# Optimization experiments

Measured on AMD Instinct MI355X. Metric: run time of the kernel, lower is better.

Reference implementation:

```python
import jax, jax.numpy as jnp
import numpy as np

EPS_OT = 0.05   # sinkhorn epsilon
ITERS = 3       # sinkhorn iterations
NH = 8          # attention heads


def _l2norm(x, axis):
    return x / jnp.maximum(jnp.linalg.norm(x, axis=axis, keepdims=True), 1e-12)


def _conv(x, w, pad):
    return jax.lax.conv_general_dilated(
        x, w, (1, 1), ((pad, pad), (pad, pad)),
        dimension_numbers=("NCHW", "OIHW", "NCHW"))


def _head(x, w1, b1, g, beta, w2, b2):
    # Conv3x3 -> BatchNorm (train-mode batch stats) -> ReLU -> Conv1x1
    h = _conv(x, w1, 1) + b1[None, :, None, None]
    mu = jnp.mean(h, (0, 2, 3), keepdims=True)
    var = jnp.var(h, (0, 2, 3), keepdims=True)
    h = jax.nn.relu((h - mu) / jnp.sqrt(var + 1e-5) * g[None, :, None, None]
                    + beta[None, :, None, None])
    return jnp.einsum("oc,bchw->bohw", w2, h) + b2[None, :, None, None]


def setup_inputs() -> dict:
    key = jax.random.key(0)
    ks = jax.random.split(key, 20)
    B, C, H, W, TD = 8, 256, 48, 48, 512
    s = 0.02
    f32 = jnp.float32
    d = {
        "img_feat": jax.random.normal(ks[0], (B, C, H, W), f32),
        "txt_feat": jax.random.normal(ks[1], (B, TD), f32),
        "density_map": jax.random.uniform(ks[2], (B, 1, H, W), f32),
        "tp_w": s * jax.random.normal(ks[3], (C, TD), f32), "tp_b": jnp.zeros((C,), f32),
        "wq": s * jax.random.normal(ks[4], (C, C), f32), "bq": jnp.zeros((C,), f32),
        "wk": s * jax.random.normal(ks[5], (C, C), f32), "bk": jnp.zeros((C,), f32),
        "wv": s * jax.random.normal(ks[6], (C, C), f32), "bv": jnp.zeros((C,), f32),
        "wo": s * jax.random.normal(ks[7], (C, C), f32), "bo": jnp.zeros((C,), f32),
        "ln_g": jnp.ones((C,), f32), "ln_b": jnp.zeros((C,), f32),
        "op_w": s * jax.random.normal(ks[8], (C, C), f32), "op_b": jnp.zeros((C,), f32),
        "h1_w": s * jax.random.normal(ks[9], (C // 2, C, 3, 3), f32), "h1_b": jnp.zeros((C // 2,), f32),
        "h_bn_g": jnp.ones((C // 2,), f32), "h_bn_b": jnp.zeros((C // 2,), f32),
        "h2_w": s * jax.random.normal(ks[10], (2, C // 2), f32), "h2_b": jnp.zeros((2,), f32),
        "v1_w": s * jax.random.normal(ks[11], (C // 2, C, 3, 3), f32), "v1_b": jnp.zeros((C // 2,), f32),
        "v_bn_g": jnp.ones((C // 2,), f32), "v_bn_b": jnp.zeros((C // 2,), f32),
        "v2_w": s * jax.random.normal(ks[12], (2, C // 2), f32), "v2_b": jnp.zeros((2,), f32),
        "temperature": 0.07 * jnp.ones((1,), f32),
        "spatial_weight": 0.1 * jnp.ones((1,), f32),
    }
    return d


def reference(img_feat, txt_feat, density_map, tp_w, tp_b, wq, bq, wk, bk,
              wv, bv, wo, bo, ln_g, ln_b, op_w, op_b, h1_w, h1_b, h_bn_g,
              h_bn_b, h2_w, h2_b, v1_w, v1_b, v_bn_g, v_bn_b, v2_w, v2_b,
              temperature, spatial_weight):
    B, C, H, W = img_feat.shape
    N = H * W
    hd = C // NH

    # ---- text projection (single text token) ----
    txt_emb = txt_feat @ tp_w.T + tp_b                      # [B,C]

    # ---- cross attention: query = pixels, key/value = 1 text token ----
    img_flat = img_feat.reshape(B, C, N).transpose(0, 2, 1)  # [B,N,C]
    q = (img_flat @ wq.T + bq).reshape(B, N, NH, hd)
    k = (txt_emb @ wk.T + bk).reshape(B, 1, NH, hd)
    v = (txt_emb @ wv.T + bv).reshape(B, 1, NH, hd)
    scores = jnp.einsum("bnhd,bkhd->bhnk", q, k) / jnp.sqrt(jnp.float32(hd))
    attn = jax.nn.softmax(scores, axis=-1)                  # ones (k len = 1)
    ctx = jnp.einsum("bhnk,bkhd->bnhd", attn, v).reshape(B, N, C)
    attn_out = ctx @ wo.T + bo

    # ---- residual + layernorm ----
    x = img_flat + attn_out
    mu = jnp.mean(x, -1, keepdims=True)
    var = jnp.var(x, -1, keepdims=True)
    source_feat = (x - mu) / jnp.sqrt(var + 1e-5) * ln_g + ln_b   # [B,N,C]
    mod_img_feat = source_feat.transpose(0, 2, 1).reshape(B, C, H, W)

    # ---- target distribution q from density map ----
    target = jax.nn.relu(density_map.reshape(B, N)) + 1e-6
    q_dist = target / jnp.sum(target, axis=1, keepdims=True)

    # ---- source distribution p from cosine similarity ----
    img_n = _l2norm(mod_img_feat, 1)                        # [B,C,H,W]
    txt_n = _l2norm(txt_emb, 1)                             # [B,C]
    cos = jnp.sum(img_n * txt_n[:, :, None, None], axis=1).reshape(B, N)
    temp = jnp.clip(temperature, 0.01, None)                # [1]
    logits = cos / temp
    mask = (cos > 0.0).astype(jnp.float32)
    shifted = logits - jnp.max(logits, axis=1, keepdims=True)
    p_un = jnp.exp(shifted) * mask + 1e-8
    p = p_un / jnp.sum(p_un, axis=1, keepdims=True)

    # ---- cost matrix: feature + spatial ----
    src_n = _l2norm(source_feat, 2)                         # [B,N,C]
    feature_cost = 1.0 - jnp.einsum("bnc,bmc->bnm", src_n, src_n)
    gy, gx = jnp.meshgrid(jnp.linspace(0.0, 1.0, H), jnp.linspace(0.0, 1.0, W),
                          indexing="ij")
    coords = jnp.stack([gy, gx], -1).reshape(N, 2)
    d2 = jnp.sum((coords[:, None, :] - coords[None, :, :]) ** 2, -1)
    spatial_cost = jnp.sqrt(jnp.maximum(d2, 0.0)) / 1.41421356  # [N,N]
    cost = feature_cost + spatial_weight * spatial_cost[None]   # [B,N,N]

    # ---- log-domain Sinkhorn ----
    log_p = jnp.log(p + 1e-12)
    log_q = jnp.log(q_dist + 1e-12)
    f = jnp.zeros_like(p)
    g = jnp.zeros_like(q_dist)
    for _ in range(ITERS):
        f = EPS_OT * (log_p - jax.scipy.special.logsumexp(
            (g[:, None, :] - cost) / EPS_OT, axis=2))
        g = EPS_OT * (log_q - jax.scipy.special.logsumexp(
            (f[:, :, None] - cost) / EPS_OT, axis=1))
    T = jnp.exp((f[:, :, None] + g[:, None, :] - cost) / EPS_OT)

    # ---- transport features: T^T @ source ----
    fused = jnp.einsum("bnm,bnc->bmc", T, source_feat)      # [B,N,C]
    fused_feat = fused.transpose(0, 2, 1).reshape(B, C, H, W)

    out_feat = img_feat + (jnp.einsum("oc,bchw->bohw", op_w, fused_feat)
                           + op_b[None, :, None, None])
    heatmap_logits = _head(out_feat, h1_w, h1_b, h_bn_g, h_bn_b, h2_w, h2_b)
    hv_logits = _head(out_feat, v1_w, v1_b, v_bn_g, v_bn_b, v2_w, v2_b)
    return out_feat, heatmap_logits, hv_logits
```

## Files before the change

### kernel.cpp

```cpp
#include <hip/hip_runtime.h>
#include <hip/hip_bf16.h>

#define NTOK 2304
#define CCH  256
#define BB   8
#define NSPL 2

typedef __attribute__((ext_vector_type(4))) float f32x4;
typedef __attribute__((ext_vector_type(8))) short s16x8;
typedef __attribute__((ext_vector_type(8))) _Float16 h16x8;
typedef unsigned short u16;
typedef unsigned char u8;

__device__ __forceinline__ u16 f2bf(float x){
  union{float f; unsigned u;} v; v.f = x;
  unsigned r = v.u + 0x7fffu + ((v.u>>16)&1u);
  return (u16)(r>>16);
}
__device__ __forceinline__ float bf2f(u16 h){
  union{float f; unsigned u;} v; v.u = ((unsigned)h)<<16; return v.f;
}

#if __has_builtin(__builtin_amdgcn_cvt_f32_fp8) && __has_builtin(__builtin_amdgcn_cvt_pk_fp8_f32)
#define HWFP8 1
#else
#define HWFP8 0
#endif

__device__ __forceinline__ u8 enc8(float z){
  union{float f; unsigned u;} a; a.f = fabsf(z) * 0x1p-120f;
  unsigned u = a.u + 0x7FFFFu + ((a.u>>20)&1u);
  unsigned b = (u>>20)&0x7Fu;
  if (b > 0x7Eu) b = 0x7Eu;
  return (u8)(b | (z<0.f ? 0x80u : 0u));
}
__device__ __forceinline__ float dec8(unsigned b){
  union{unsigned u; float f;} w;
  w.u = ((b&0x80u)<<24) | ((b&0x7Fu)<<20);
  return w.f * 0x1p120f;
}

#if HWFP8
__device__ __forceinline__ float DEC8(unsigned w, int e){
  switch(e & 3){
    case 0:  return __builtin_amdgcn_cvt_f32_fp8((int)w, 0);
    case 1:  return __builtin_amdgcn_cvt_f32_fp8((int)w, 1);
    case 2:  return __builtin_amdgcn_cvt_f32_fp8((int)w, 2);
    default: return __builtin_amdgcn_cvt_f32_fp8((int)w, 3);
  }
}
__device__ __forceinline__ unsigned pack4(float z0,float z1,float z2,float z3){
  int v = __builtin_amdgcn_cvt_pk_fp8_f32(z0, z1, 0, false);
  v = __builtin_amdgcn_cvt_pk_fp8_f32(z2, z3, v, true);
  return (unsigned)v;
}
#else
__device__ __forceinline__ float DEC8(unsigned w, int e){
  return dec8((w>>(8*(e&3)))&0xFFu);
}
__device__ __forceinline__ unsigned pack4(float z0,float z1,float z2,float z3){
  return (unsigned)enc8(z0) | ((unsigned)enc8(z1)<<8) |
         ((unsigned)enc8(z2)<<16) | ((unsigned)enc8(z3)<<24);
}
#endif

__device__ __forceinline__ int swz512(int row, int b){ return row*512 + (b ^ ((row&7)<<4)); }
__device__ __forceinline__ int swz128(int row, int b){ return row*128 + (b ^ ((row&7)<<4)); }
__device__ __forceinline__ int swz64 (int row, int b){ return row*64  + (b ^ ((row&3)<<4)); }

__device__ __forceinline__ void gl_lds16(const void* g, void* l){
  __builtin_amdgcn_global_load_lds(
      (const __attribute__((address_space(1))) unsigned int*)g,
      (__attribute__((address_space(3))) unsigned int*)l, 16, 0, 0);
}

struct CanonArgs {
  const void* src[31];
  int n[31];
  int off[31];
};

__global__ void k_detect(const u16* probe, int* flag){
  if (threadIdx.x==0){
    int cnt=0;
    for (int i=0;i<16;++i){
      unsigned e = (probe[2*i]>>7)&0xFFu;
      if (e>=100u && e<=140u) ++cnt;
    }
    *flag = (cnt>=14)?1:0;
  }
}

__global__ __launch_bounds__(256) void k_canon(CanonArgs a, float* dst, const int* flag, int nt){
  int t = blockIdx.y;
  if (t>=nt) return;
  int n = a.n[t];
  const void* s = a.src[t];
  float* d = dst + a.off[t];
  bool isbf = (*flag)!=0;
  int n4 = n >> 2;
  for (int i = blockIdx.x*256+threadIdx.x; i < n4; i += gridDim.x*256){
    if (isbf){
      ushort4 v = ((const ushort4*)s)[i];
      float4 o; o.x=bf2f(v.x); o.y=bf2f(v.y); o.z=bf2f(v.z); o.w=bf2f(v.w);
      ((float4*)d)[i] = o;
    } else {
      ((float4*)d)[i] = ((const float4*)s)[i];
    }
  }
  int base = n4<<2;
  int rem = n - base;
  int i = blockIdx.x*256+threadIdx.x;
  if (i < rem)
    d[base+i] = isbf ? bf2f(((const u16*)s)[base+i]) : ((const float*)s)[base+i];
}

__global__ __launch_bounds__(256) void k_zero(float* p, int n4){
  int i = blockIdx.x*256+threadIdx.x;
  if (i < n4) ((float4*)p)[i] = (float4){0.f,0.f,0.f,0.f};
}

__global__ __launch_bounds__(256) void k_txt(const float* txt, const float* tpw, const float* tpb,
    const float* wv, const float* bv, const float* wo, const float* bo, float* TXTN, float* AVEC){
  int b=blockIdx.x, t=threadIdx.x;
  __shared__ float sT[512];
  __shared__ float sE[256];
  __shared__ float sV[256];
  __shared__ float red[4];
  sT[t]      = txt[b*512+t];
  sT[t+256]  = txt[b*512+256+t];
  __syncthreads();
  float acc = tpb[t];
  const float* wr = tpw + (size_t)t*512;
  for (int k=0;k<512;++k) acc = fmaf(sT[k], wr[k], acc);
  sE[t] = acc;
  float ss = acc*acc;
  for (int d=1; d<64; d<<=1) ss += __shfl_xor(ss, d);
  if ((t&63)==0) red[t>>6] = ss;
  __syncthreads();
  float nrm = sqrtf(red[0]+red[1]+red[2]+red[3]);
  TXTN[b*256+t] = acc / fmaxf(nrm, 1e-12f);
  float av = bv[t];
  const float* wvr = wv + (size_t)t*256;
  for (int k=0;k<256;++k) av = fmaf(sE[k], wvr[k], av);
  sV[t] = av;
  __syncthreads();
  float ao = bo[t];
  const float* wor = wo + (size_t)t*256;
  for (int k=0;k<256;++k) ao = fmaf(sV[k], wor[k], ao);
  AVEC[b*256+t] = ao;
}

__global__ __launch_bounds__(256) void k_lnfuse(const float* img, const float* AVEC, const float* lng,
    const float* lnb, const float* TXTN, u16* SF, u16* SN, float* COS){
  int b=blockIdx.y, n0=blockIdx.x*32, t=threadIdx.x;
  __shared__ float xt[32][256];
  float av = AVEC[b*256+t];
  const float* ip = img + ((size_t)b*256 + t)*NTOK + n0;
  #pragma unroll
  for (int j4=0;j4<8;++j4){
    float4 v = *(const float4*)(ip + j4*4);
    xt[j4*4+0][t]=v.x+av; xt[j4*4+1][t]=v.y+av; xt[j4*4+2][t]=v.z+av; xt[j4*4+3][t]=v.w+av;
  }
  int wv_=t>>6, l=t&63;
  float lg[4], lb[4], tn[4];
  #pragma unroll
  for (int k=0;k<4;++k){ lg[k]=lng[l+64*k]; lb[k]=lnb[l+64*k]; tn[k]=TXTN[b*256+l+64*k]; }
  __syncthreads();
  for (int rr=0; rr<8; ++rr){
    int j = wv_*8+rr; int n = n0+j;
    float x[4]; float s=0.f, ss=0.f;
    #pragma unroll
    for (int k=0;k<4;++k){ float v=xt[j][l+64*k]; x[k]=v; s+=v; ss=fmaf(v,v,ss); }
    for (int d=1; d<64; d<<=1){ s += __shfl_xor(s,d); ss += __shfl_xor(ss,d); }
    float mu = s*(1.f/256.f);
    float var = ss*(1.f/256.f) - mu*mu;
    float rstd = rsqrtf(fmaxf(var,0.f)+1e-5f);
    float y[4]; float sy=0.f;
    #pragma unroll
    for (int k=0;k<4;++k){ y[k] = fmaf((x[k]-mu)*rstd, lg[k], lb[k]); sy = fmaf(y[k],y[k],sy); }
    for (int d=1; d<64; d<<=1) sy += __shfl_xor(sy,d);
    float rn = 1.f/fmaxf(sqrtf(sy),1e-12f);
    float cp = 0.f;
    size_t base = ((size_t)b*NTOK + n)*CCH;
    #pragma unroll
    for (int k=0;k<4;++k){
      float sv = y[k]*rn;
      SF[base + l+64*k] = f2bf(y[k]);
      SN[base + l+64*k] = f2bf(sv);
      cp = fmaf(sv, tn[k], cp);
    }
    for (int d=1; d<64; d<<=1) cp += __shfl_xor(cp,d);
    if (l==0) COS[b*NTOK+n] = cp;
  }
}

__global__ __launch_bounds__(256) void k_pqred(const float* COS, const float* den, const float* tmpp, float* PQS){
  int b=blockIdx.x, t=threadIdx.x;
  __shared__ float red[256];
  float temp = fmaxf(tmpp[0], 0.01f);
  float mx = -1e30f;
  for (int n=t; n<NTOK; n+=256) mx = fmaxf(mx, COS[b*NTOK+n]);
  red[t]=mx; __syncthreads();
  for (int o=128;o>0;o>>=1){ if (t<o) red[t]=fmaxf(red[t],red[t+o]); __syncthreads(); }
  float maxc = red[0]; __syncthreads();
  float sp=0.f, st=0.f;
  for (int n=t; n<NTOK; n+=256){
    float cv = COS[b*NTOK+n];
    sp += __expf((cv-maxc)/temp)*((cv>0.f)?1.f:0.f)+1e-8f;
    float dv = den[b*NTOK+n];
    st += fmaxf(dv,0.f)+1e-6f;
  }
  red[t]=sp; __syncthreads();
  for (int o=128;o>0;o>>=1){ if (t<o) red[t]+=red[t+o]; __syncthreads(); }
  sp = red[0]; __syncthreads();
  red[t]=st; __syncthreads();
  for (int o=128;o>0;o>>=1){ if (t<o) red[t]+=red[t+o]; __syncthreads(); }
  if (t==0){ PQS[b*4]=maxc; PQS[b*4+1]=sp; PQS[b*4+2]=red[0]; }
}

__global__ __launch_bounds__(256) void k_pqelem(const float* COS, const float* den, const float* tmpp,
    const float* PQS, float* LOGP, float* LOGQ, float* GV, float* CY, float* CX){
  int idx = blockIdx.x*256+threadIdx.x;
  float temp = fmaxf(tmpp[0], 0.01f);
  if (idx < BB*NTOK){
    int b = idx / NTOK;
    float maxc = PQS[b*4], sp = PQS[b*4+1], st = PQS[b*4+2];
    float cv = COS[idx];
    float pu = __expf((cv-maxc)/temp)*((cv>0.f)?1.f:0.f)+1e-8f;
    LOGP[idx] = logf(pu/sp + 1e-12f);
    float dv = den[idx];
    LOGQ[idx] = logf((fmaxf(dv,0.f)+1e-6f)/st + 1e-12f);
    GV[idx] = 0.f;
  }
  if (idx < NTOK){
    int h = idx/48, w = idx - h*48;
    CY[idx] = (float)h*(1.f/47.f);
    CX[idx] = (float)w*(1.f/47.f);
  }
}

__global__ __launch_bounds__(256) void k_packw(const float* h1w, const float* v1w, u16* W2P){
  int idx = blockIdx.x*256+threadIdx.x;
  int kc = idx >> 14;
  int rem = idx & 16383;
  int o = rem >> 6;
  int cl = rem & 63;
  int tap = kc >> 2;
  int c = ((kc&3)<<6) + cl;
  int head = o >> 7, oc = o & 127;
  const float* src = head ? v1w : h1w;
  W2P[idx] = f2bf(src[(oc*256 + c)*9 + tap]);
}

__global__ __launch_bounds__(256) void k_trans(const u16* SF, u16* SFT){
  int n0 = blockIdx.x*64, c0 = blockIdx.y*64, b = blockIdx.z;
  __shared__ u16 tl[64][68];
  int t = threadIdx.x;
  int nl = t>>3, c8 = (t&7)*8;
  #pragma unroll
  for (int p=0;p<2;++p){
    int n = nl + p*32;
    s16x8 v = *(const s16x8*)(SF + ((size_t)(b*NTOK + n0+n)*CCH + c0 + c8));
    #pragma unroll
    for (int e=0;e<8;++e) tl[c8+e][n] = (u16)v[e];
  }
  __syncthreads();
  int cl = t>>3, n8 = (t&7)*8;
  #pragma unroll
  for (int p=0;p<2;++p){
    int c = cl + p*32;
    union{ s16x8 v; u16 us[8]; } pk;
    #pragma unroll
    for (int e=0;e<8;++e){ int s = n8+e; pk.us[e] = tl[c][((s&3)<<4) | (s>>2)]; }
    *(s16x8*)(SFT + ((size_t)(b*CCH + c0+c)*NTOK + n0 + n8)) = pk.v;
  }
}

__global__ __launch_bounds__(256, 4) void k_cost(const u16* SN, const float* CY, const float* CX,
    const float* swp, u8* Z, float* PZ, int b_base){
  int zb = blockIdx.z, b = b_base + zb;
  int i0 = blockIdx.x*64, by = blockIdx.y, j0b = by*256;
  const u16* SNb = SN + (size_t)b*NTOK*CCH;
  u8* Zb = Z + (size_t)zb*NTOK*NTOK;
  __shared__ __align__(16) char Bs[64*512];
  int tid=threadIdx.x, w=tid>>6, l=tid&63, g4=l>>4, lc=l&15;
  float spw = swp[0]*(20.0f/1.41421356f);
  const u16* Arow = SNb + (size_t)(i0 + w*16 + lc)*CCH + g4*8;
  s16x8 af[8];
  #pragma unroll
  for (int ks=0; ks<8; ++ks) af[ks] = *(const s16x8*)(Arow + ks*32);
  int mrow = w*16 + g4*4;
  float cyi[4], cxi[4];
  #pragma unroll
  for (int r=0;r<4;++r){ int i = i0+mrow+r; cyi[r]=CY[i]; cxi[r]=CX[i]; }
  float Srow[4] = {0.f,0.f,0.f,0.f};
  for (int js=0; js<4; ++js){
    int j0 = j0b + js*64;
    __syncthreads();
    #pragma unroll
    for (int u=0; u<8; ++u){
      int row = u*8 + w*2 + (l>>5);
      int src = ((l&31)*16) ^ ((row&7)<<4);
      gl_lds16((const char*)(SNb + (size_t)(j0+row)*CCH) + src, Bs + u*4096 + w*1024);
    }
    __syncthreads();
    f32x4 acc[4];
    #pragma unroll
    for (int cf=0;cf<4;++cf) acc[cf] = (f32x4){0.f,0.f,0.f,0.f};
    #pragma unroll
    for (int ks=0; ks<8; ++ks){
      int kb = ks*64 + g4*16;
      #pragma unroll
      for (int cf=0; cf<4; ++cf){
        s16x8 bb = *(const s16x8*)(Bs + swz512(cf*16+lc, kb));
        acc[cf] = __builtin_amdgcn_mfma_f32_16x16x32_bf16(af[ks], bb, acc[cf], 0,0,0);
      }
    }
    float zf[4][4];
    #pragma unroll
    for (int cf=0; cf<4; ++cf){
      int j = j0 + cf*16 + lc;
      float cyj = CY[j], cxj = CX[j];
      #pragma unroll
      for (int r=0;r<4;++r){
        float dy = cyi[r]-cyj, dx = cxi[r]-cxj;
        zf[cf][r] = (acc[cf][r]-1.0f)*20.0f - spw*sqrtf(fmaf(dy,dy,dx*dx));
      }
    }
    size_t zrow = (size_t)(i0+mrow)*NTOK + j0 + lc*4;
    #pragma unroll
    for (int r=0;r<4;++r){
      unsigned pw = pack4(zf[0][r], zf[1][r], zf[2][r], zf[3][r]);
      Srow[r] += __expf(DEC8(pw,0)) + __expf(DEC8(pw,1))
               + __expf(DEC8(pw,2)) + __expf(DEC8(pw,3));
      *(unsigned*)(Zb + zrow + (size_t)r*NTOK) = pw;
    }
  }
  #pragma unroll
  for (int r=0;r<4;++r){
    float s = Srow[r];
    s += __shfl_xor(s,1); s += __shfl_xor(s,2); s += __shfl_xor(s,4); s += __shfl_xor(s,8);
    if (lc==0) PZ[(size_t)(zb*NTOK + i0 + mrow + r)*9 + by] = s;
  }
}

__global__ __launch_bounds__(256) void k_sinkred(const float* PZ, const float* LOGP, float* FV,
    int b_base, int zcnt){
  int idx = blockIdx.x*256 + threadIdx.x;
  if (idx >= zcnt*NTOK) return;
  int zb = idx / NTOK, row = idx - zb*NTOK, b = b_base + zb;
  const float* p = PZ + (size_t)idx*9;
  float s = 0.f;
  #pragma unroll
  for (int k=0;k<9;++k) s += p[k];
  FV[b*NTOK+row] = 0.05f*(LOGP[b*NTOK+row] - logf(s));
}

__global__ __launch_bounds__(256) void k_sinkZ(const u8* Z, const float* addv,
    const float* basev, float* outv, int b_base){
  int zb = blockIdx.y, b = b_base + zb, i0 = blockIdx.x*32;
  __shared__ float fs[NTOK];
  __shared__ float wm[4];
  int t = threadIdx.x;
  for (int j=t; j<NTOK; j+=256){
    int p = j & 63, tt = ((p&3)<<4) | (p>>2);
    fs[j] = addv[b*NTOK + (j & ~63) + tt]*20.f;
  }
  __syncthreads();
  float m = -1e30f;
  for (int j=t; j<NTOK; j+=256) m = fmaxf(m, fs[j]);
  #pragma unroll
  for (int d=1; d<64; d<<=1) m = fmaxf(m, __shfl_xor(m, d));
  if ((t&63)==0) wm[t>>6] = m;
  __syncthreads();
  float C = fmaxf(fmaxf(wm[0],wm[1]), fmaxf(wm[2],wm[3]));
  int rl = t>>3, q = t&7;
  int row = i0 + rl;
  const u8* zr = Z + ((size_t)zb*NTOK + row)*NTOK;
  float S = 0.f;
  for (int c0 = q*32; c0 < NTOK; c0 += 256){
    uint4 zA = *(const uint4*)(zr + c0);
    uint4 zB = *(const uint4*)(zr + c0 + 16);
    unsigned wd[8] = {zA.x,zA.y,zA.z,zA.w, zB.x,zB.y,zB.z,zB.w};
    float s32 = 0.f;
    #pragma unroll
    for (int k=0;k<8;++k)
      #pragma unroll
      for (int e=0;e<4;++e)
        s32 += __expf(fs[c0 + k*4 + e] + DEC8(wd[k], e) - C);
    S += s32;
  }
  #pragma unroll
  for (int d=1; d<8; d<<=1) S += __shfl_xor(S, d);
  if (q==0)
    outv[b*NTOK+row] = 0.05f*(basev[b*NTOK+row] - (C + logf(S)));
}

__global__ __launch_bounds__(256, 3) void k_applyT(const u8* Z, const u16* SFT, const float* FVv,
    const float* GVv, float* FUF, int b_base){
  int zb = blockIdx.z, b = b_base + zb, m0 = blockIdx.x*64;
  int sp = blockIdx.y;
  int nbeg = sp*(NTOK/NSPL), nend = nbeg + (NTOK/NSPL);
  __shared__ __align__(16) char WtL[64*128];
  __shared__ __align__(16) char BL[256*128];
  __shared__ float gs[64];
  __shared__ float sfv[NTOK/NSPL];
  int tid=threadIdx.x, w=tid>>6, l=tid&63, g4=l>>4, lc=l&15;
  if (tid<64) gs[tid] = GVv[b*NTOK+m0+tid]*20.f;
  const float* Fv = FVv + b*NTOK;
  for (int j=tid; j<NTOK/NSPL; j+=256){
    int jj = nbeg + j;
    int p = jj & 63, tt = ((p&3)<<4) | (p>>2);
    sfv[j] = Fv[(jj & ~63) + tt]*20.f;
  }
  const u8* Zb = Z + ((size_t)zb*NTOK + m0)*NTOK;
  const u16* SFTb = SFT + (size_t)b*CCH*NTOK;
  f32x4 acc[4][4];
  #pragma unroll
  for (int mf=0;mf<4;++mf)
    #pragma unroll
    for (int cf=0;cf<4;++cf) acc[mf][cf] = (f32x4){0.f,0.f,0.f,0.f};
  int zm = tid>>2, zq = (tid&3)*16;
  int lrow = l>>3;
  int lsrc = ((l&7)*16) ^ (lrow<<4);
  uint4 zwc = *(const uint4*)(Zb + (size_t)zm*NTOK + nbeg + zq);
  for (int n0=nbeg; n0<nend; n0+=64){
    __syncthreads();
    int nn = (n0+64 < nend) ? n0+64 : nbeg;
    uint4 zwn = *(const uint4*)(Zb + (size_t)zm*NTOK + nn + zq);
    #pragma unroll
    for (int u=0; u<8; ++u){
      int row = w*64 + u*8 + lrow;
      gl_lds16((const char*)(SFTb + (size_t)row*NTOK) + n0*2 + lsrc,
               BL + (w*64 + u*8)*128);
    }
    {
      float g20 = gs[zm];
      unsigned wd[4] = {zwc.x, zwc.y, zwc.z, zwc.w};
      union{ s16x8 v; u16 us[8]; } w0, w1;
      int sbase = n0 - nbeg + zq;
      #pragma unroll
      for (int col=0; col<16; ++col){
        float val = __expf(sfv[sbase+col] + g20 + DEC8(wd[col>>2], col&3));
        if (col < 8) w0.us[col] = f2bf(val); else w1.us[col-8] = f2bf(val);
      }
      *(s16x8*)(WtL + swz128(zm, zq*2)) = w0.v;
      *(s16x8*)(WtL + swz128(zm, zq*2+16)) = w1.v;
    }
    __syncthreads();
    #pragma unroll
    for (int kk=0; kk<2; ++kk){
      s16x8 a[4];
      #pragma unroll
      for (int mf=0;mf<4;++mf) a[mf] = *(const s16x8*)(WtL + swz128(mf*16+lc, kk*64 + g4*16));
      #pragma unroll
      for (int cf=0; cf<4; ++cf){
        s16x8 bb = *(const s16x8*)(BL + swz128(w*64+cf*16+lc, kk*64 + g4*16));
        #pragma unroll
        for (int mf=0; mf<4; ++mf)
          acc[mf][cf] = __builtin_amdgcn_mfma_f32_16x16x32_bf16(a[mf], bb, acc[mf][cf], 0,0,0);
      }
    }
    zwc = zwn;
  }
  float* FUb = FUF + (size_t)b*NTOK*CCH;
  #pragma unroll
  for (int mf=0; mf<4; ++mf)
    #pragma unroll
    for (int cf=0; cf<4; ++cf)
      #pragma unroll
      for (int r=0;r<4;++r){
        int m = m0 + mf*16 + g4*4 + r;
        int c = w*64 + cf*16 + lc;
        atomicAdd(&FUb[(size_t)m*CCH + c], acc[mf][cf][r]);
      }
}

__global__ __launch_bounds__(256) void k_opgemm(const float* FUF, const float* opw, const float* opb,
    const float* img, float* dout, u16* OFN){
  int b=blockIdx.y, n0=blockIdx.x*64;
  __shared__ __align__(16) char Am[64*512];
  __shared__ __align__(16) char Bw[256*64];
  int tid=threadIdx.x, w=tid>>6, l=tid&63, g4=l>>4, lc=l&15;
  const float* FUb = FUF + (size_t)b*NTOK*CCH;
  for (int ch=tid; ch<64*32; ch+=256){
    int r=ch>>5, c8=(ch&31)*8;
    const float* fp = FUb + (size_t)(n0+r)*CCH + c8;
    float4 v0 = *(const float4*)fp;
    float4 v1 = *(const float4*)(fp+4);
    union { s16x8 v; u16 us[8]; } pk;
    pk.us[0]=f2bf(v0.x); pk.us[1]=f2bf(v0.y); pk.us[2]=f2bf(v0.z); pk.us[3]=f2bf(v0.w);
    pk.us[4]=f2bf(v1.x); pk.us[5]=f2bf(v1.y); pk.us[6]=f2bf(v1.z); pk.us[7]=f2bf(v1.w);
    *(s16x8*)(Am + swz512(r, c8*2)) = pk.v;
  }
  f32x4 acc[4][4];
  #pragma unroll
  for (int mf=0;mf<4;++mf)
    #pragma unroll
    for (int cf=0;cf<4;++cf) acc[mf][cf] = (f32x4){0.f,0.f,0.f,0.f};
  for (int ks=0; ks<8; ++ks){
    __syncthreads();
    {
      int o = tid;
      const float* wr = opw + (size_t)o*CCH + ks*32;
      #pragma unroll
      for (int u=0; u<4; ++u){
        float4 v0 = *(const float4*)(wr + u*8);
        float4 v1 = *(const float4*)(wr + u*8 + 4);
        union { s16x8 v; u16 us[8]; } pk;
        pk.us[0]=f2bf(v0.x); pk.us[1]=f2bf(v0.y); pk.us[2]=f2bf(v0.z); pk.us[3]=f2bf(v0.w);
        pk.us[4]=f2bf(v1.x); pk.us[5]=f2bf(v1.y); pk.us[6]=f2bf(v1.z); pk.us[7]=f2bf(v1.w);
        *(s16x8*)(Bw + swz64(o, u*16)) = pk.v;
      }
    }
    __syncthreads();
    #pragma unroll
    for (int mf=0; mf<4; ++mf){
      s16x8 a = *(const s16x8*)(Am + swz512(mf*16+lc, (ks*32+g4*8)*2));
      #pragma unroll
      for (int cf=0; cf<4; ++cf){
        int o = w*64+cf*16+lc;
        s16x8 bb = *(const s16x8*)(Bw + swz64(o, g4*16));
        acc[mf][cf] = __builtin_amdgcn_mfma_f32_16x16x32_bf16(a, bb, acc[mf][cf], 0,0,0);
      }
    }
  }
  #pragma unroll
  for (int mf=0; mf<4; ++mf){
    int nl = mf*16 + g4*4; int n = n0+nl;
    #pragma unroll
    for (int cf=0; cf<4; ++cf){
      int o = w*64+cf*16+lc;
      float ob = opb[o];
      const float* ip = img + ((size_t)b*CCH + o)*NTOK + n;
      float4 im = *(const float4*)ip;
      float o0 = acc[mf][cf][0]+ob+im.x;
      float o1 = acc[mf][cf][1]+ob+im.y;
      float o2 = acc[mf][cf][2]+ob+im.z;
      float o3 = acc[mf][cf][3]+ob+im.w;
      float4 st; st.x=o0; st.y=o1; st.z=o2; st.w=o3;
      *(float4*)(dout + ((size_t)b*CCH+o)*NTOK + n) = st;
      u16* ofp = OFN + ((size_t)b*NTOK + n)*CCH + o;
      ofp[0]=f2bf(o0); ofp[CCH]=f2bf(o1); ofp[2*CCH]=f2bf(o2); ofp[3*CCH]=f2bf(o3);
    }
  }
}

__global__ __launch_bounds__(256, 2) void k_conv2(const u16* OFN, const u16* W2P,
    const float* h1b, const float* v1b, u16* H1, u16* H2){
  int b = blockIdx.y, n0 = blockIdx.x*64;
  __shared__ __align__(16) char As[64*128];
  __shared__ __align__(16) char Ws[2][256*128];
  int tid=threadIdx.x, w=tid>>6, l=tid&63, g4=l>>4, lc=l&15;
  int ar = tid>>2, aseg = (tid&3)*16;
  int arow = n0 + ar;
  int hr = arow/48, wc = arow - hr*48;
  const u16* Ob = OFN + (size_t)b*NTOK*CCH;
  int wrow = tid>>3;
  int wsrc = ((tid&7)*16) ^ ((wrow&7)<<4);
  const char* Wbase = (const char*)W2P;
  f32x4 acc[4][4];
  #pragma unroll
  for (int mf=0;mf<4;++mf)
    #pragma unroll
    for (int of=0;of<4;++of) acc[mf][of] = (f32x4){0.f,0.f,0.f,0.f};
  auto STAGEW = [&](int kc, int buf){
    const char* src = Wbase + (size_t)kc*32768;
    #pragma unroll
    for (int u=0; u<8; ++u)
      gl_lds16(src + (size_t)(u*32 + wrow)*128 + wsrc, Ws[buf] + u*4096 + w*1024);
  };
  auto LOADA = [&](int kc, s16x8& ra0, s16x8& ra1){
    int tap = kc>>2, cq = (kc&3)*64;
    int kh = tap/3;
    int dh = kh-1, dw = (tap-kh*3)-1;
    bool val = ((unsigned)(hr+dh) < 48u) && ((unsigned)(wc+dw) < 48u);
    ra0 = (s16x8){0,0,0,0,0,0,0,0}; ra1 = ra0;
    if (val){
      const u16* ap = Ob + (size_t)(arow + dh*48 + dw)*CCH + cq + aseg;
      ra0 = *(const s16x8*)ap;
      ra1 = *(const s16x8*)(ap+8);
    }
  };
  s16x8 a0, a1, na0, na1;
  STAGEW(0, 0);
  LOADA(0, a0, a1);
  for (int kc=0; kc<36; ++kc){
    int cur = kc & 1;
    __builtin_amdgcn_s_barrier();
    __builtin_amdgcn_sched_barrier(0);
    if (kc+1 < 36){
      STAGEW(kc+1, cur^1);
      LOADA(kc+1, na0, na1);
    }
    *(s16x8*)(As + swz128(ar, aseg*2))    = a0;
    *(s16x8*)(As + swz128(ar, aseg*2+16)) = a1;
    asm volatile("s_waitcnt lgkmcnt(0)" ::: "memory");
    __builtin_amdgcn_s_barrier();
    __builtin_amdgcn_sched_barrier(0);
    #pragma unroll
    for (int ks=0; ks<2; ++ks){
      s16x8 af[4];
      #pragma unroll
      for (int mf=0;mf<4;++mf) af[mf] = *(const s16x8*)(As + swz128(mf*16+lc, ks*64 + g4*16));
      #pragma unroll
      for (int of=0; of<4; ++of){
        s16x8 bf = *(const s16x8*)(Ws[cur] + swz128(w*64+of*16+lc, ks*64 + g4*16));
        #pragma unroll
        for (int mf=0; mf<4; ++mf)
          acc[mf][of] = __builtin_amdgcn_mfma_f32_16x16x32_bf16(af[mf], bf, acc[mf][of], 0,0,0);
      }
    }
    a0 = na0; a1 = na1;
  }
  #pragma unroll
  for (int of=0; of<4; ++of){
    int o = w*64 + of*16 + lc;
    int head = o>>7, oc = o&127;
    float bias = (head? v1b : h1b)[oc];
    u16* Hh = head? H2 : H1;
    #pragma unroll
    for (int mf=0; mf<4; ++mf){
      #pragma unroll
      for (int r=0;r<4;++r){
        int n = n0 + mf*16 + g4*4 + r;
        Hh[((size_t)b*NTOK+n)*128 + oc] = f2bf(acc[mf][of][r] + bias);
      }
    }
  }
}

__global__ __launch_bounds__(128) void k_stats(const u16* H1, const u16* H2, float* PART){
  int head=blockIdx.y, blk=blockIdx.x, t=threadIdx.x;
  const u16* Hh = head? H2:H1;
  float s=0.f, ss=0.f;
  size_t r0 = (size_t)blk*288;
  for (int r=0;r<288;++r){
    float v = bf2f(Hh[(r0+r)*128 + t]);
    s += v; ss = fmaf(v,v,ss);
  }
  PART[((head*64+blk)*128+t)*2]   = s;
  PART[((head*64+blk)*128+t)*2+1] = ss;
}

__global__ __launch_bounds__(128) void k_statr(const float* PART, const float* hbg, const float* hbb,
    const float* vbg, const float* vbb, float* BNS){
  int head=blockIdx.x, t=threadIdx.x;
  float s=0.f, ss=0.f;
  for (int blk=0;blk<64;++blk){
    s  += PART[((head*64+blk)*128+t)*2];
    ss += PART[((head*64+blk)*128+t)*2+1];
  }
  float mean = s*(1.f/18432.f);
  float var = ss*(1.f/18432.f) - mean*mean;
  var = fmaxf(var, 0.f);
  const float* g  = head? vbg:hbg;
  const float* be = head? vbb:hbb;
  float sc = g[t]/sqrtf(var+1e-5f);
  BNS[(head*128+t)*2]   = sc;
  BNS[(head*128+t)*2+1] = be[t] - mean*sc;
}

__global__ __launch_bounds__(128) void k_fin(const u16* H1, const u16* H2, const float* BNS,
    const float* h2w, const float* h2b, const float* v2w, const float* v2b, float* dout){
  int head = blockIdx.z, b = blockIdx.y, n0 = blockIdx.x*128, t=threadIdx.x;
  const u16* Hh = head? H2:H1;
  const float* w2 = head? v2w:h2w;
  const float* b2 = head? v2b:h2b;
  __shared__ u16 tile[128][130];
  __shared__ float sc[128], bi[128], wa[128], wb[128];
  sc[t]=BNS[(head*128+t)*2]; bi[t]=BNS[(head*128+t)*2+1];
  wa[t]=w2[t]; wb[t]=w2[128+t];
  for (int r=0;r<128;++r) tile[r][t] = Hh[((size_t)b*NTOK+n0+r)*128 + t];
  __syncthreads();
  float a0=b2[0], a1=b2[1];
  for (int ch=0; ch<128; ++ch){
    float v = fmaf(bf2f(tile[t][ch]), sc[ch], bi[ch]);
    v = fmaxf(v, 0.f);
    a0 = fmaf(wa[ch], v, a0);
    a1 = fmaf(wb[ch], v, a1);
  }
  size_t base = (size_t)8*256*2304 + (size_t)head*36864 + (size_t)b*2*2304 + n0 + t;
  dout[base]        = a0;
  dout[base+2304]   = a1;
}

extern "C" void kernel_launch(void* const* d_in, const int* in_sizes, int n_in,
                              void* d_out, int out_size, void* d_ws, size_t ws_size,
                              hipStream_t stream){
  (void)out_size;
  long off[31]; long tot=0;
  int ni = n_in < 31 ? n_in : 31;
  for (int i=0;i<ni;++i){ off[i]=tot; tot += ((long)in_sizes[i]+63)&~63L; }
  char* ws = (char*)d_ws;
  size_t pos = 0;
  auto alloc = [&](size_t bytes)->char*{
    char* p = ws+pos; pos = (pos + bytes + 255) & ~(size_t)255; return p; };
  int*   FLAG = (int*)alloc(256);
  float* TXTN = (float*)alloc(8*256*4);
  float* AVEC = (float*)alloc(8*256*4);
  float* COS  = (float*)alloc(8*2304*4);
  float* LOGP = (float*)alloc(8*2304*4);
  float* LOGQ = (float*)alloc(8*2304*4);
  float* FV   = (float*)alloc(8*2304*4);
  float* GV   = (float*)alloc(8*2304*4);
  float* CY   = (float*)alloc(2304*4);
  float* CX   = (float*)alloc(2304*4);
  float* PQS  = (float*)alloc(8*4*4);
  float* PART = (float*)alloc(2*64*128*2*4);
  float* BNS  = (float*)alloc(2*128*2*4);
  float* PZ   = (float*)alloc((size_t)8*2304*9*4);
  u16* W2P = (u16*)alloc((size_t)36*256*64*2);
  u16* SF  = (u16*)alloc((size_t)8*2304*256*2);
  u16* SN  = (u16*)alloc((size_t)8*2304*256*2);
  u16* SFT = (u16*)alloc((size_t)8*2304*256*2);
  float* FUF = (float*)alloc((size_t)8*2304*256*4);
  u16* OFN = (u16*)alloc((size_t)8*2304*256*2);
  u16* H1  = (u16*)alloc((size_t)8*2304*128*2);
  u16* H2  = (u16*)alloc((size_t)8*2304*128*2);
  float* canon = (float*)alloc((size_t)tot*4);
  size_t zslice = (size_t)NTOK*NTOK;
  int zsl = (pos + 8*zslice + 256 <= ws_size) ? 8 : 1;
  u8* Z = (u8*)alloc((size_t)zsl*zslice);

  k_detect<<<1,64,0,stream>>>((const u16*)d_in[1], FLAG);
  CanonArgs ca;
  for (int i=0;i<ni;++i){ ca.src[i]=d_in[i]; ca.n[i]=in_sizes[i]; ca.off[i]=(int)off[i]; }
  k_canon<<<dim3(512,(unsigned)ni),256,0,stream>>>(ca, canon, FLAG, ni);
  k_zero<<<4608,256,0,stream>>>(FUF, 8*2304*256/4);

  const float* c_img = canon+off[0];
  const float* c_txt = canon+off[1];
  const float* c_den = canon+off[2];
  const float* c_tpw = canon+off[3];
  const float* c_tpb = canon+off[4];
  const float* c_wv  = canon+off[9];
  const float* c_bv  = canon+off[10];
  const float* c_wo  = canon+off[11];
  const float* c_bo  = canon+off[12];
  const float* c_lng = canon+off[13];
  const float* c_lnb = canon+off[14];
  const float* c_opw = canon+off[15];
  const float* c_opb = canon+off[16];
  const float* c_h1w = canon+off[17];
  const float* c_h1b = canon+off[18];
  const float* c_hbg = canon+off[19];
  const float* c_hbb = canon+off[20];
  const float* c_h2w = canon+off[21];
  const float* c_h2b = canon+off[22];
  const float* c_v1w = canon+off[23];
  const float* c_v1b = canon+off[24];
  const float* c_vbg = canon+off[25];
  const float* c_vbb = canon+off[26];
  const float* c_v2w = canon+off[27];
  const float* c_v2b = canon+off[28];
  const float* c_tmp = canon+off[29];
  const float* c_sw  = canon+off[30];

  k_txt<<<8,256,0,stream>>>(c_txt, c_tpw, c_tpb, c_wv, c_bv, c_wo, c_bo, TXTN, AVEC);
  k_lnfuse<<<dim3(72,8),256,0,stream>>>(c_img, AVEC, c_lng, c_lnb, TXTN, SF, SN, COS);
  k_pqred<<<8,256,0,stream>>>(COS, c_den, c_tmp, PQS);
  k_pqelem<<<80,256,0,stream>>>(COS, c_den, c_tmp, PQS, LOGP, LOGQ, GV, CY, CX);
  k_packw<<<2304,256,0,stream>>>(c_h1w, c_v1w, W2P);
  k_trans<<<dim3(36,4,8),256,0,stream>>>(SF, SFT);

  if (zsl == 8){
    k_cost<<<dim3(36,9,8),256,0,stream>>>(SN, CY, CX, c_sw, Z, PZ, 0);
    k_sinkred<<<72,256,0,stream>>>(PZ, LOGP, FV, 0, 8);
    for (int it=0; it<3; ++it){
      if (it>0) k_sinkZ<<<dim3(72,8),256,0,stream>>>(Z, GV, LOGP, FV, 0);
      k_sinkZ<<<dim3(72,8),256,0,stream>>>(Z, FV, LOGQ, GV, 0);
    }
    k_applyT<<<dim3(36,NSPL,8),256,0,stream>>>(Z, SFT, FV, GV, FUF, 0);
  } else {
    for (int bi=0; bi<8; ++bi){
      k_cost<<<dim3(36,9,1),256,0,stream>>>(SN, CY, CX, c_sw, Z, PZ, bi);
      k_sinkred<<<9,256,0,stream>>>(PZ, LOGP, FV, bi, 1);
      for (int it=0; it<3; ++it){
        if (it>0) k_sinkZ<<<dim3(72,1),256,0,stream>>>(Z, GV, LOGP, FV, bi);
        k_sinkZ<<<dim3(72,1),256,0,stream>>>(Z, FV, LOGQ, GV, bi);
      }
      k_applyT<<<dim3(36,NSPL,1),256,0,stream>>>(Z, SFT, FV, GV, FUF, bi);
    }
  }

  k_opgemm<<<dim3(36,8),256,0,stream>>>(FUF, c_opw, c_opb, c_img, (float*)d_out, OFN);
  k_conv2<<<dim3(36,8),256,0,stream>>>(OFN, W2P, c_h1b, c_v1b, H1, H2);
  k_stats<<<dim3(64,2),128,0,stream>>>(H1, H2, PART);
  k_statr<<<2,128,0,stream>>>(PART, c_hbg, c_hbb, c_vbg, c_vbb, BNS);
  k_fin<<<dim3(18,8,2),128,0,stream>>>(H1, H2, BNS, c_h2w, c_h2b, c_v2w, c_v2b, (float*)d_out);
}
```

Measured before the change: 385.9 us.

## Overlap cost-tile staging with epilogue and tabulate spatial distance costs

New measurement: 407.8 us. +5.7%, slower.

```diff
diff --git a/kernel.cpp b/kernel.cpp
--- a/kernel.cpp
+++ b/kernel.cpp
@@ -220,7 +220,7 @@
 }
 
 __global__ __launch_bounds__(256) void k_pqelem(const float* COS, const float* den, const float* tmpp,
-    const float* PQS, float* LOGP, float* LOGQ, float* GV, float* CY, float* CX){
+    const float* swp, const float* PQS, float* LOGP, float* LOGQ, float* GV, u16* PJ, float* SPT){
   int idx = blockIdx.x*256+threadIdx.x;
   float temp = fmaxf(tmpp[0], 0.01f);
   if (idx < BB*NTOK){
@@ -235,8 +235,13 @@
   }
   if (idx < NTOK){
     int h = idx/48, w = idx - h*48;
-    CY[idx] = (float)h*(1.f/47.f);
-    CX[idx] = (float)w*(1.f/47.f);
+    PJ[idx] = (u16)(h*95 + w);
+  }
+  if (idx < 9025){
+    int dh = idx/95 - 47, dw = idx - (idx/95)*95 - 47;
+    float spw = swp[0]*(20.0f/1.41421356f);
+    float dy = (float)dh*(1.f/47.f), dx = (float)dw*(1.f/47.f);
+    SPT[idx] = spw*sqrtf(fmaf(dy,dy,dx*dx));
   }
 }
 
@@ -277,34 +282,36 @@
   }
 }
 
-__global__ __launch_bounds__(256, 4) void k_cost(const u16* SN, const float* CY, const float* CX,
-    const float* swp, u8* Z, float* PZ, int b_base){
+__global__ __launch_bounds__(256, 5) void k_cost(const u16* SN, const u16* PJ, const float* SPT,
+    u8* Z, float* PZ, int b_base){
   int zb = blockIdx.z, b = b_base + zb;
   int i0 = blockIdx.x*64, by = blockIdx.y, j0b = by*256;
   const u16* SNb = SN + (size_t)b*NTOK*CCH;
   u8* Zb = Z + (size_t)zb*NTOK*NTOK;
   __shared__ __align__(16) char Bs[64*512];
   int tid=threadIdx.x, w=tid>>6, l=tid&63, g4=l>>4, lc=l&15;
-  float spw = swp[0]*(20.0f/1.41421356f);
   const u16* Arow = SNb + (size_t)(i0 + w*16 + lc)*CCH + g4*8;
   s16x8 af[8];
   #pragma unroll
   for (int ks=0; ks<8; ++ks) af[ks] = *(const s16x8*)(Arow + ks*32);
   int mrow = w*16 + g4*4;
-  float cyi[4], cxi[4];
-  #pragma unroll
-  for (int r=0;r<4;++r){ int i = i0+mrow+r; cyi[r]=CY[i]; cxi[r]=CX[i]; }
+  int ipi[4];
+  #pragma unroll
+  for (int r=0;r<4;++r) ipi[r] = (int)PJ[i0+mrow+r] + 4512;
   float Srow[4] = {0.f,0.f,0.f,0.f};
-  for (int js=0; js<4; ++js){
+  auto STAGE = [&](int js){
     int j0 = j0b + js*64;
-    __syncthreads();
     #pragma unroll
     for (int u=0; u<8; ++u){
       int row = u*8 + w*2 + (l>>5);
       int src = ((l&31)*16) ^ ((row&7)<<4);
       gl_lds16((const char*)(SNb + (size_t)(j0+row)*CCH) + src, Bs + u*4096 + w*1024);
     }
-    __syncthreads();
+  };
+  STAGE(0);
+  __syncthreads();
+  for (int js=0; js<4; ++js){
+    int j0 = j0b + js*64;
     f32x4 acc[4];
     #pragma unroll
     for (int cf=0;cf<4;++cf) acc[cf] = (f32x4){0.f,0.f,0.f,0.f};
@@ -317,15 +324,20 @@
         acc[cf] = __builtin_amdgcn_mfma_f32_16x16x32_bf16(af[ks], bb, acc[cf], 0,0,0);
       }
     }
+    __builtin_amdgcn_sched_barrier(0);
+    __builtin_amdgcn_s_barrier();
+    __builtin_amdgcn_sched_barrier(0);
+    if (js < 3) STAGE(js+1);
+    __builtin_amdgcn_sched_barrier(0);
     float zf[4][4];
     #pragma unroll
     for (int cf=0; cf<4; ++cf){
       int j = j0 + cf*16 + lc;
-      float cyj = CY[j], cxj = CX[j];
+      int pjj = (int)PJ[j];
       #pragma unroll
       for (int r=0;r<4;++r){
-        float dy = cyi[r]-cyj, dx = cxi[r]-cxj;
-        zf[cf][r] = (acc[cf][r]-1.0f)*20.0f - spw*sqrtf(fmaf(dy,dy,dx*dx));
+        float sp = SPT[ipi[r] - pjj];
+        zf[cf][r] = (acc[cf][r]-1.0f)*20.0f - sp;
       }
     }
     size_t zrow = (size_t)(i0+mrow)*NTOK + j0 + lc*4;
@@ -336,6 +348,9 @@
                + __expf(DEC8(pw,2)) + __expf(DEC8(pw,3));
       *(unsigned*)(Zb + zrow + (size_t)r*NTOK) = pw;
     }
+    __builtin_amdgcn_sched_barrier(0);
+    __builtin_amdgcn_s_barrier();
+    __builtin_amdgcn_sched_barrier(0);
   }
   #pragma unroll
   for (int r=0;r<4;++r){
@@ -375,6 +390,9 @@
   if ((t&63)==0) wm[t>>6] = m;
   __syncthreads();
   float C = fmaxf(fmaxf(wm[0],wm[1]), fmaxf(wm[2],wm[3]));
+  __syncthreads();
+  for (int j=t; j<NTOK; j+=256) fs[j] -= C;
+  __syncthreads();
   int rl = t>>3, q = t&7;
   int row = i0 + rl;
   const u8* zr = Z + ((size_t)zb*NTOK + row)*NTOK;
@@ -388,7 +406,7 @@
     for (int k=0;k<8;++k)
       #pragma unroll
       for (int e=0;e<4;++e)
-        s32 += __expf(fs[c0 + k*4 + e] + DEC8(wd[k], e) - C);
+        s32 += __expf(fs[c0 + k*4 + e] + DEC8(wd[k], e));
     S += s32;
   }
   #pragma unroll
@@ -705,8 +723,8 @@
   float* LOGQ = (float*)alloc(8*2304*4);
   float* FV   = (float*)alloc(8*2304*4);
   float* GV   = (float*)alloc(8*2304*4);
-  float* CY   = (float*)alloc(2304*4);
-  float* CX   = (float*)alloc(2304*4);
+  u16*   PJ   = (u16*)alloc(2304*2);
+  float* SPT  = (float*)alloc(9025*4);
   float* PQS  = (float*)alloc(8*4*4);
   float* PART = (float*)alloc(2*64*128*2*4);
   float* BNS  = (float*)alloc(2*128*2*4);
@@ -761,12 +779,12 @@
   k_txt<<<8,256,0,stream>>>(c_txt, c_tpw, c_tpb, c_wv, c_bv, c_wo, c_bo, TXTN, AVEC);
   k_lnfuse<<<dim3(72,8),256,0,stream>>>(c_img, AVEC, c_lng, c_lnb, TXTN, SF, SN, COS);
   k_pqred<<<8,256,0,stream>>>(COS, c_den, c_tmp, PQS);
-  k_pqelem<<<80,256,0,stream>>>(COS, c_den, c_tmp, PQS, LOGP, LOGQ, GV, CY, CX);
+  k_pqelem<<<80,256,0,stream>>>(COS, c_den, c_tmp, c_sw, PQS, LOGP, LOGQ, GV, PJ, SPT);
   k_packw<<<2304,256,0,stream>>>(c_h1w, c_v1w, W2P);
   k_trans<<<dim3(36,4,8),256,0,stream>>>(SF, SFT);
 
   if (zsl == 8){
-    k_cost<<<dim3(36,9,8),256,0,stream>>>(SN, CY, CX, c_sw, Z, PZ, 0);
+    k_cost<<<dim3(36,9,8),256,0,stream>>>(SN, PJ, SPT, Z, PZ, 0);
     k_sinkred<<<72,256,0,stream>>>(PZ, LOGP, FV, 0, 8);
     for (int it=0; it<3; ++it){
       if (it>0) k_sinkZ<<<dim3(72,8),256,0,stream>>>(Z, GV, LOGP, FV, 0);
@@ -775,7 +793,7 @@
     k_applyT<<<dim3(36,NSPL,8),256,0,stream>>>(Z, SFT, FV, GV, FUF, 0);
   } else {
     for (int bi=0; bi<8; ++bi){
-      k_cost<<<dim3(36,9,1),256,0,stream>>>(SN, CY, CX, c_sw, Z, PZ, bi);
+      k_cost<<<dim3(36,9,1),256,0,stream>>>(SN, PJ, SPT, Z, PZ, bi);
       k_sinkred<<<9,256,0,stream>>>(PZ, LOGP, FV, bi, 1);
       for (int it=0; it<3; ++it){
         if (it>0) k_sinkZ<<<dim3(72,1),256,0,stream>>>(Z, GV, LOGP, FV, bi);
```
